# Kernel tuning notes

Hardware: AMD Instinct MI355X
Metric: run time of the kernel (lower is better)

Reference implementation:

```python
import jax, jax.numpy as jnp
import numpy as np


def setup_inputs() -> dict:
    key = jax.random.key(0)
    k1, k2 = jax.random.split(key)
    set1 = jax.random.normal(k1, (8192, 256), dtype=jnp.float32)
    set2 = jax.random.normal(k2, (8192, 256), dtype=jnp.float32)
    return {"set1": set1, "set2": set2}


def reference(set1, set2):
    # Pairwise Euclidean distances via the Gram trick:
    sq1 = jnp.sum(set1 * set1, axis=-1)  # [N]
    sq2 = jnp.sum(set2 * set2, axis=-1)  # [M]
    gram = jnp.einsum('nd,md->nm', set1, set2)  # [N,M]
    d2 = sq1[:, None] + sq2[None, :] - 2.0 * gram
    d = jnp.sqrt(jnp.maximum(d2, 0.0))  # clamp tiny negatives from roundoff
    term_1 = jnp.mean(jnp.min(d, axis=1))  # for each point in set1, nearest in set2
    term_2 = jnp.mean(jnp.min(d, axis=0))  # for each point in set2, nearest in set1
    return term_1 + term_2
```

## Files before the change

### kernel.cpp

```cpp
#include <hip/hip_runtime.h>

#define N_PTS 8192
#define D_DIM 256
#define BT 128
#define BK 32
#define INF_BITS 0x7F800000u

typedef __attribute__((ext_vector_type(8))) short short8;
typedef __attribute__((ext_vector_type(4))) float f32x4;

__device__ __forceinline__ void gload_lds16(const ushort* g, ushort* l) {
    __builtin_amdgcn_global_load_lds(
        (const __attribute__((address_space(1))) void*)g,
        (__attribute__((address_space(3))) void*)l, 16, 0, 0);
}

__device__ __forceinline__ ushort f2bf(float x) {
    unsigned u = __float_as_uint(x);
    return (ushort)((u + 0x7FFFu + ((u >> 16) & 1u)) >> 16);
}

__global__ void convert_kernel(const float* __restrict__ s1,
                               const float* __restrict__ s2,
                               ushort* __restrict__ b1,
                               ushort* __restrict__ b2) {
    const int half = N_PTS * D_DIM;
    int i = (blockIdx.x * 256 + threadIdx.x) * 8;
    const float* src; ushort* dst; int off;
    if (i < half) { src = s1; dst = b1; off = i; }
    else          { src = s2; dst = b2; off = i - half; }
    float4 v0 = *(const float4*)(src + off);
    float4 v1 = *(const float4*)(src + off + 4);
    ushort4 o0 = { f2bf(v0.x), f2bf(v0.y), f2bf(v0.z), f2bf(v0.w) };
    ushort4 o1 = { f2bf(v1.x), f2bf(v1.y), f2bf(v1.z), f2bf(v1.w) };
    *(ushort4*)(dst + off)     = o0;
    *(ushort4*)(dst + off + 4) = o1;
}

__global__ void sqnorm_kernel(const float* __restrict__ set1,
                              const float* __restrict__ set2,
                              float* __restrict__ sq1,
                              float* __restrict__ sq2) {
    int wave = threadIdx.x >> 6;
    int lane = threadIdx.x & 63;
    int row = blockIdx.x * 4 + wave;
    const float* src; float* dst; int r;
    if (row < N_PTS) { src = set1; dst = sq1; r = row; }
    else             { src = set2; dst = sq2; r = row - N_PTS; }
    float4 v = ((const float4*)(src + (size_t)r * D_DIM))[lane];
    float s = v.x * v.x + v.y * v.y + v.z * v.z + v.w * v.w;
    #pragma unroll
    for (int off = 32; off > 0; off >>= 1) s += __shfl_down(s, off, 64);
    if (lane == 0) dst[r] = s;
}

__global__ void init_kernel(unsigned int* __restrict__ rowmin2,
                            unsigned int* __restrict__ colmin2) {
    int i = blockIdx.x * blockDim.x + threadIdx.x;
    if (i < N_PTS) { rowmin2[i] = INF_BITS; colmin2[i] = INF_BITS; }
}

__global__ __launch_bounds__(256) void tile_kernel(
    const ushort* __restrict__ B1, const ushort* __restrict__ B2,
    const float* __restrict__ sq1, const float* __restrict__ sq2,
    unsigned int* __restrict__ rowmin2, unsigned int* __restrict__ colmin2) {
    __shared__ ushort As[BT * BK] __attribute__((aligned(16)));
    __shared__ ushort Bs[BT * BK] __attribute__((aligned(16)));
    __shared__ unsigned int rs[BT];
    __shared__ unsigned int cs[BT];

    const int tid  = threadIdx.x;
    const int lane = tid & 63;
    const int w    = tid >> 6;
    const int quad = lane >> 4;
    const int c    = lane & 15;
    const int n_off = (w >> 1) * 64;
    const int m_off = (w & 1) * 64;
    const int n0 = blockIdx.y * BT;
    const int m0 = blockIdx.x * BT;

    if (tid < BT) { rs[tid] = INF_BITS; cs[tid] = INF_BITS; }

    f32x4 acc[4][4];
    #pragma unroll
    for (int ti = 0; ti < 4; ti++)
        #pragma unroll
        for (int tj = 0; tj < 4; tj++) acc[ti][tj] = (f32x4){0.f, 0.f, 0.f, 0.f};

    for (int k0 = 0; k0 < D_DIM; k0 += BK) {
        #pragma unroll
        for (int ch = 0; ch < 2; ch++) {
            int idx = ch * 256 + tid;
            int row = idx >> 2;
            int c4  = idx & 3;
            gload_lds16(B1 + (size_t)(n0 + row) * D_DIM + k0 + c4 * 8,
                        &As[(idx & ~63) * 8]);
            gload_lds16(B2 + (size_t)(m0 + row) * D_DIM + k0 + c4 * 8,
                        &Bs[(idx & ~63) * 8]);
        }
        __syncthreads();

        short8 a[4], b[4];
        #pragma unroll
        for (int ti = 0; ti < 4; ti++)
            a[ti] = *(const short8*)&As[(n_off + ti * 16 + c) * BK + quad * 8];
        #pragma unroll
        for (int tj = 0; tj < 4; tj++)
            b[tj] = *(const short8*)&Bs[(m_off + tj * 16 + c) * BK + quad * 8];
        #pragma unroll
        for (int ti = 0; ti < 4; ti++)
            #pragma unroll
            for (int tj = 0; tj < 4; tj++)
                acc[ti][tj] = __builtin_amdgcn_mfma_f32_16x16x32_bf16(
                    a[ti], b[tj], acc[ti][tj], 0, 0, 0);
        __syncthreads();
    }

    float sqn[4][4], sqm[4];
    #pragma unroll
    for (int ti = 0; ti < 4; ti++)
        #pragma unroll
        for (int r = 0; r < 4; r++)
            sqn[ti][r] = sq1[n0 + n_off + ti * 16 + quad * 4 + r];
    #pragma unroll
    for (int tj = 0; tj < 4; tj++)
        sqm[tj] = sq2[m0 + m_off + tj * 16 + c];

    float rmin[4][4], cmin[4];
    #pragma unroll
    for (int ti = 0; ti < 4; ti++)
        #pragma unroll
        for (int r = 0; r < 4; r++) rmin[ti][r] = __uint_as_float(INF_BITS);
    #pragma unroll
    for (int tj = 0; tj < 4; tj++) cmin[tj] = __uint_as_float(INF_BITS);

    #pragma unroll
    for (int ti = 0; ti < 4; ti++)
        #pragma unroll
        for (int tj = 0; tj < 4; tj++)
            #pragma unroll
            for (int r = 0; r < 4; r++) {
                float d2 = fmaxf(sqn[ti][r] + sqm[tj] - 2.f * acc[ti][tj][r], 0.f);
                rmin[ti][r] = fminf(rmin[ti][r], d2);
                cmin[tj]    = fminf(cmin[tj], d2);
            }

    #pragma unroll
    for (int m = 1; m <= 8; m <<= 1)
        #pragma unroll
        for (int ti = 0; ti < 4; ti++)
            #pragma unroll
            for (int r = 0; r < 4; r++)
                rmin[ti][r] = fminf(rmin[ti][r], __shfl_xor(rmin[ti][r], m, 64));
    #pragma unroll
    for (int m = 16; m <= 32; m <<= 1)
        #pragma unroll
        for (int tj = 0; tj < 4; tj++)
            cmin[tj] = fminf(cmin[tj], __shfl_xor(cmin[tj], m, 64));

    if (c == 0) {
        #pragma unroll
        for (int ti = 0; ti < 4; ti++)
            #pragma unroll
            for (int r = 0; r < 4; r++)
                atomicMin(&rs[n_off + ti * 16 + quad * 4 + r],
                          __float_as_uint(rmin[ti][r]));
    }
    if (quad == 0) {
        #pragma unroll
        for (int tj = 0; tj < 4; tj++)
            atomicMin(&cs[m_off + tj * 16 + c], __float_as_uint(cmin[tj]));
    }
    __syncthreads();
    if (tid < BT) atomicMin(&rowmin2[n0 + tid], rs[tid]);
    else          atomicMin(&colmin2[m0 + tid - BT], cs[tid - BT]);
}

__global__ void reduce_kernel(const unsigned int* __restrict__ rowmin2,
                              const unsigned int* __restrict__ colmin2,
                              float* __restrict__ out) {
    float s = 0.f;
    for (int i = threadIdx.x; i < N_PTS; i += blockDim.x) {
        s += sqrtf(__uint_as_float(rowmin2[i]));
        s += sqrtf(__uint_as_float(colmin2[i]));
    }
    #pragma unroll
    for (int off = 32; off > 0; off >>= 1) s += __shfl_down(s, off, 64);
    __shared__ float ws[4];
    int lane = threadIdx.x & 63, wave = threadIdx.x >> 6;
    if (lane == 0) ws[wave] = s;
    __syncthreads();
    if (threadIdx.x == 0) out[0] = (ws[0] + ws[1] + ws[2] + ws[3]) / (float)N_PTS;
}

extern "C" void kernel_launch(void* const* d_in, const int* in_sizes, int n_in,
                              void* d_out, int out_size, void* d_ws, size_t ws_size,
                              hipStream_t stream) {
    const float* set1 = (const float*)d_in[0];
    const float* set2 = (const float*)d_in[1];
    float* out = (float*)d_out;

    unsigned int* rowmin2 = (unsigned int*)d_ws;
    unsigned int* colmin2 = rowmin2 + N_PTS;
    float* sq1 = (float*)(colmin2 + N_PTS);
    float* sq2 = sq1 + N_PTS;
    ushort* b1 = (ushort*)(sq2 + N_PTS);
    ushort* b2 = b1 + (size_t)N_PTS * D_DIM;

    init_kernel<<<(N_PTS + 255) / 256, 256, 0, stream>>>(rowmin2, colmin2);
    sqnorm_kernel<<<(2 * N_PTS) / 4, 256, 0, stream>>>(set1, set2, sq1, sq2);
    convert_kernel<<<(2 * N_PTS * D_DIM) / (256 * 8), 256, 0, stream>>>(
        set1, set2, b1, b2);
    tile_kernel<<<dim3(N_PTS / BT, N_PTS / BT), 256, 0, stream>>>(
        b1, b2, sq1, sq2, rowmin2, colmin2);
    reduce_kernel<<<1, 256, 0, stream>>>(rowmin2, colmin2, out);
}
```

Before: 139.7 us.

## Fuse prep kernels, enlarge swizzled GEMM tiles, fold final reduction into last block

Merges the conversion, squared-norm and min-init kernels into one prep pass, cutting launches and a second read of the fp32 inputs. The tile kernel grows to 256x128 tiles with BK=64 and an XOR-swizzled LDS layout, meant to avoid bank conflicts and raise reuse per loaded element. The separate reduce kernel is replaced by a last-block-done counter that does the final sqrt-mean inside the tile kernel. Costs are higher register pressure from 32 accumulators per wave (launch bounds set to 2 blocks) and a serial tail in the last block.

```diff
diff --git a/kernel.cpp b/kernel.cpp
--- a/kernel.cpp
+++ b/kernel.cpp
@@ -2,8 +2,10 @@
 
 #define N_PTS 8192
 #define D_DIM 256
-#define BT 128
-#define BK 32
+#define BN 256
+#define BM 128
+#define BK 64
+#define NBLK ((N_PTS / BN) * (N_PTS / BM))
 #define INF_BITS 0x7F800000u
 
 typedef __attribute__((ext_vector_type(8))) short short8;
@@ -20,177 +22,181 @@
     return (ushort)((u + 0x7FFFu + ((u >> 16) & 1u)) >> 16);
 }
 
-__global__ void convert_kernel(const float* __restrict__ s1,
-                               const float* __restrict__ s2,
-                               ushort* __restrict__ b1,
-                               ushort* __restrict__ b2) {
+__global__ void prep_kernel(const float* __restrict__ s1, const float* __restrict__ s2,
+                            ushort* __restrict__ b1, ushort* __restrict__ b2,
+                            float* __restrict__ sq1, float* __restrict__ sq2,
+                            unsigned* __restrict__ rowmin2, unsigned* __restrict__ colmin2,
+                            unsigned* __restrict__ counter) {
     const int half = N_PTS * D_DIM;
-    int i = (blockIdx.x * 256 + threadIdx.x) * 8;
-    const float* src; ushort* dst; int off;
-    if (i < half) { src = s1; dst = b1; off = i; }
-    else          { src = s2; dst = b2; off = i - half; }
+    int t = blockIdx.x * 256 + threadIdx.x;
+    int e = t * 8;
+    bool first = e < half;
+    const float* src = first ? s1 : s2;
+    ushort* dst = first ? b1 : b2;
+    int off = first ? e : e - half;
     float4 v0 = *(const float4*)(src + off);
     float4 v1 = *(const float4*)(src + off + 4);
+    float s = v0.x * v0.x + v0.y * v0.y + v0.z * v0.z + v0.w * v0.w
+            + v1.x * v1.x + v1.y * v1.y + v1.z * v1.z + v1.w * v1.w;
     ushort4 o0 = { f2bf(v0.x), f2bf(v0.y), f2bf(v0.z), f2bf(v0.w) };
     ushort4 o1 = { f2bf(v1.x), f2bf(v1.y), f2bf(v1.z), f2bf(v1.w) };
     *(ushort4*)(dst + off)     = o0;
     *(ushort4*)(dst + off + 4) = o1;
-}
-
-__global__ void sqnorm_kernel(const float* __restrict__ set1,
-                              const float* __restrict__ set2,
-                              float* __restrict__ sq1,
-                              float* __restrict__ sq2) {
-    int wave = threadIdx.x >> 6;
-    int lane = threadIdx.x & 63;
-    int row = blockIdx.x * 4 + wave;
-    const float* src; float* dst; int r;
-    if (row < N_PTS) { src = set1; dst = sq1; r = row; }
-    else             { src = set2; dst = sq2; r = row - N_PTS; }
-    float4 v = ((const float4*)(src + (size_t)r * D_DIM))[lane];
-    float s = v.x * v.x + v.y * v.y + v.z * v.z + v.w * v.w;
-    #pragma unroll
-    for (int off = 32; off > 0; off >>= 1) s += __shfl_down(s, off, 64);
-    if (lane == 0) dst[r] = s;
-}
-
-__global__ void init_kernel(unsigned int* __restrict__ rowmin2,
-                            unsigned int* __restrict__ colmin2) {
-    int i = blockIdx.x * blockDim.x + threadIdx.x;
-    if (i < N_PTS) { rowmin2[i] = INF_BITS; colmin2[i] = INF_BITS; }
-}
-
-__global__ __launch_bounds__(256) void tile_kernel(
+    #pragma unroll
+    for (int m = 1; m <= 16; m <<= 1) s += __shfl_xor(s, m, 64);
+    int sub = threadIdx.x & 31;
+    int row = off >> 8;
+    if (sub == 0) (first ? sq1 : sq2)[row] = s;
+    if (sub == 1) (first ? rowmin2 : colmin2)[row] = INF_BITS;
+    if (t == 0) *counter = 0;
+}
+
+__global__ __launch_bounds__(256, 2) void tile_kernel(
     const ushort* __restrict__ B1, const ushort* __restrict__ B2,
     const float* __restrict__ sq1, const float* __restrict__ sq2,
-    unsigned int* __restrict__ rowmin2, unsigned int* __restrict__ colmin2) {
-    __shared__ ushort As[BT * BK] __attribute__((aligned(16)));
-    __shared__ ushort Bs[BT * BK] __attribute__((aligned(16)));
-    __shared__ unsigned int rs[BT];
-    __shared__ unsigned int cs[BT];
+    unsigned* __restrict__ rowmin2, unsigned* __restrict__ colmin2,
+    unsigned* __restrict__ counter, float* __restrict__ out) {
+    __shared__ ushort As[BN * BK] __attribute__((aligned(16)));
+    __shared__ ushort Bs[BM * BK] __attribute__((aligned(16)));
+    __shared__ unsigned rs[BN];
+    __shared__ unsigned cs[BM];
+    __shared__ unsigned s_last;
+    __shared__ float wsum[4];
 
     const int tid  = threadIdx.x;
     const int lane = tid & 63;
     const int w    = tid >> 6;
     const int quad = lane >> 4;
     const int c    = lane & 15;
-    const int n_off = (w >> 1) * 64;
+    const int n_off = (w >> 1) * 128;
     const int m_off = (w & 1) * 64;
-    const int n0 = blockIdx.y * BT;
-    const int m0 = blockIdx.x * BT;
-
-    if (tid < BT) { rs[tid] = INF_BITS; cs[tid] = INF_BITS; }
-
-    f32x4 acc[4][4];
-    #pragma unroll
-    for (int ti = 0; ti < 4; ti++)
+    const int n0 = blockIdx.y * BN;
+    const int m0 = blockIdx.x * BM;
+
+    rs[tid] = INF_BITS;
+    if (tid < BM) cs[tid] = INF_BITS;
+
+    f32x4 acc[8][4];
+    #pragma unroll
+    for (int ti = 0; ti < 8; ti++)
         #pragma unroll
         for (int tj = 0; tj < 4; tj++) acc[ti][tj] = (f32x4){0.f, 0.f, 0.f, 0.f};
 
     for (int k0 = 0; k0 < D_DIM; k0 += BK) {
         #pragma unroll
-        for (int ch = 0; ch < 2; ch++) {
-            int idx = ch * 256 + tid;
-            int row = idx >> 2;
-            int c4  = idx & 3;
-            gload_lds16(B1 + (size_t)(n0 + row) * D_DIM + k0 + c4 * 8,
+        for (int r = 0; r < 8; r++) {
+            int idx = r * 256 + tid;
+            int row = idx >> 3;
+            int gc  = (idx & 7) ^ (row & 7);
+            gload_lds16(B1 + (size_t)(n0 + row) * D_DIM + k0 + gc * 8,
                         &As[(idx & ~63) * 8]);
-            gload_lds16(B2 + (size_t)(m0 + row) * D_DIM + k0 + c4 * 8,
+        }
+        #pragma unroll
+        for (int r = 0; r < 4; r++) {
+            int idx = r * 256 + tid;
+            int row = idx >> 3;
+            int gc  = (idx & 7) ^ (row & 7);
+            gload_lds16(B2 + (size_t)(m0 + row) * D_DIM + k0 + gc * 8,
                         &Bs[(idx & ~63) * 8]);
         }
         __syncthreads();
 
-        short8 a[4], b[4];
-        #pragma unroll
-        for (int ti = 0; ti < 4; ti++)
-            a[ti] = *(const short8*)&As[(n_off + ti * 16 + c) * BK + quad * 8];
-        #pragma unroll
-        for (int tj = 0; tj < 4; tj++)
-            b[tj] = *(const short8*)&Bs[(m_off + tj * 16 + c) * BK + quad * 8];
-        #pragma unroll
-        for (int ti = 0; ti < 4; ti++)
-            #pragma unroll
-            for (int tj = 0; tj < 4; tj++)
-                acc[ti][tj] = __builtin_amdgcn_mfma_f32_16x16x32_bf16(
-                    a[ti], b[tj], acc[ti][tj], 0, 0, 0);
+        #pragma unroll
+        for (int kk = 0; kk < 2; kk++) {
+            short8 a[8], b[4];
+            #pragma unroll
+            for (int ti = 0; ti < 8; ti++) {
+                int row = n_off + ti * 16 + c;
+                int ch  = (kk * 4 + quad) ^ (row & 7);
+                a[ti] = *(const short8*)&As[row * BK + ch * 8];
+            }
+            #pragma unroll
+            for (int tj = 0; tj < 4; tj++) {
+                int row = m_off + tj * 16 + c;
+                int ch  = (kk * 4 + quad) ^ (row & 7);
+                b[tj] = *(const short8*)&Bs[row * BK + ch * 8];
+            }
+            #pragma unroll
+            for (int ti = 0; ti < 8; ti++)
+                #pragma unroll
+                for (int tj = 0; tj < 4; tj++)
+                    acc[ti][tj] = __builtin_amdgcn_mfma_f32_16x16x32_bf16(
+                        a[ti], b[tj], acc[ti][tj], 0, 0, 0);
+        }
         __syncthreads();
     }
 
-    float sqn[4][4], sqm[4];
-    #pragma unroll
-    for (int ti = 0; ti < 4; ti++)
-        #pragma unroll
-        for (int r = 0; r < 4; r++)
-            sqn[ti][r] = sq1[n0 + n_off + ti * 16 + quad * 4 + r];
-    #pragma unroll
-    for (int tj = 0; tj < 4; tj++)
-        sqm[tj] = sq2[m0 + m_off + tj * 16 + c];
-
-    float rmin[4][4], cmin[4];
-    #pragma unroll
-    for (int ti = 0; ti < 4; ti++)
-        #pragma unroll
-        for (int r = 0; r < 4; r++) rmin[ti][r] = __uint_as_float(INF_BITS);
+    float sqm[4];
+    #pragma unroll
+    for (int tj = 0; tj < 4; tj++) sqm[tj] = sq2[m0 + m_off + tj * 16 + c];
+    float cmin[4];
     #pragma unroll
     for (int tj = 0; tj < 4; tj++) cmin[tj] = __uint_as_float(INF_BITS);
 
     #pragma unroll
-    for (int ti = 0; ti < 4; ti++)
-        #pragma unroll
-        for (int tj = 0; tj < 4; tj++)
+    for (int ti = 0; ti < 8; ti++) {
+        float4 sqn = *(const float4*)&sq1[n0 + n_off + ti * 16 + quad * 4];
+        float rmin[4] = { __uint_as_float(INF_BITS), __uint_as_float(INF_BITS),
+                          __uint_as_float(INF_BITS), __uint_as_float(INF_BITS) };
+        #pragma unroll
+        for (int tj = 0; tj < 4; tj++) {
+            float sn[4] = { sqn.x, sqn.y, sqn.z, sqn.w };
             #pragma unroll
             for (int r = 0; r < 4; r++) {
-                float d2 = fmaxf(sqn[ti][r] + sqm[tj] - 2.f * acc[ti][tj][r], 0.f);
-                rmin[ti][r] = fminf(rmin[ti][r], d2);
-                cmin[tj]    = fminf(cmin[tj], d2);
+                float d2 = fmaxf(sn[r] + sqm[tj] - 2.f * acc[ti][tj][r], 0.f);
+                rmin[r]  = fminf(rmin[r], d2);
+                cmin[tj] = fminf(cmin[tj], d2);
             }
-
-    #pragma unroll
-    for (int m = 1; m <= 8; m <<= 1)
-        #pragma unroll
-        for (int ti = 0; ti < 4; ti++)
+        }
+        #pragma unroll
+        for (int m = 1; m <= 8; m <<= 1)
             #pragma unroll
             for (int r = 0; r < 4; r++)
-                rmin[ti][r] = fminf(rmin[ti][r], __shfl_xor(rmin[ti][r], m, 64));
+                rmin[r] = fminf(rmin[r], __shfl_xor(rmin[r], m, 64));
+        if (c == 0) {
+            #pragma unroll
+            for (int r = 0; r < 4; r++)
+                atomicMin(&rs[n_off + ti * 16 + quad * 4 + r], __float_as_uint(rmin[r]));
+        }
+    }
     #pragma unroll
     for (int m = 16; m <= 32; m <<= 1)
         #pragma unroll
         for (int tj = 0; tj < 4; tj++)
             cmin[tj] = fminf(cmin[tj], __shfl_xor(cmin[tj], m, 64));
-
-    if (c == 0) {
-        #pragma unroll
-        for (int ti = 0; ti < 4; ti++)
-            #pragma unroll
-            for (int r = 0; r < 4; r++)
-                atomicMin(&rs[n_off + ti * 16 + quad * 4 + r],
-                          __float_as_uint(rmin[ti][r]));
-    }
     if (quad == 0) {
         #pragma unroll
         for (int tj = 0; tj < 4; tj++)
             atomicMin(&cs[m_off + tj * 16 + c], __float_as_uint(cmin[tj]));
     }
     __syncthreads();
-    if (tid < BT) atomicMin(&rowmin2[n0 + tid], rs[tid]);
-    else          atomicMin(&colmin2[m0 + tid - BT], cs[tid - BT]);
-}
-
-__global__ void reduce_kernel(const unsigned int* __restrict__ rowmin2,
-                              const unsigned int* __restrict__ colmin2,
-                              float* __restrict__ out) {
-    float s = 0.f;
-    for (int i = threadIdx.x; i < N_PTS; i += blockDim.x) {
-        s += sqrtf(__uint_as_float(rowmin2[i]));
-        s += sqrtf(__uint_as_float(colmin2[i]));
-    }
-    #pragma unroll
-    for (int off = 32; off > 0; off >>= 1) s += __shfl_down(s, off, 64);
-    __shared__ float ws[4];
-    int lane = threadIdx.x & 63, wave = threadIdx.x >> 6;
-    if (lane == 0) ws[wave] = s;
+
+    atomicMin(&rowmin2[n0 + tid], rs[tid]);
+    if (tid < BM) atomicMin(&colmin2[m0 + tid], cs[tid]);
+
+    __threadfence();
     __syncthreads();
-    if (threadIdx.x == 0) out[0] = (ws[0] + ws[1] + ws[2] + ws[3]) / (float)N_PTS;
+    if (tid == 0) s_last = (atomicAdd(counter, 1) == NBLK - 1) ? 1u : 0u;
+    __syncthreads();
+    if (s_last) {
+        __threadfence();
+        const unsigned* mins = rowmin2;
+        float s = 0.f;
+        for (int base = 0; base < 2 * N_PTS; base += 2048) {
+            unsigned v[8];
+            #pragma unroll
+            for (int j = 0; j < 8; j++)
+                v[j] = __hip_atomic_load(&mins[base + j * 256 + tid],
+                                         __ATOMIC_RELAXED, __HIP_MEMORY_SCOPE_AGENT);
+            #pragma unroll
+            for (int j = 0; j < 8; j++) s += sqrtf(__uint_as_float(v[j]));
+        }
+        #pragma unroll
+        for (int off = 32; off > 0; off >>= 1) s += __shfl_down(s, off, 64);
+        if (lane == 0) wsum[w] = s;
+        __syncthreads();
+        if (tid == 0) out[0] = (wsum[0] + wsum[1] + wsum[2] + wsum[3]) / (float)N_PTS;
+    }
 }
 
 extern "C" void kernel_launch(void* const* d_in, const int* in_sizes, int n_in,
@@ -200,18 +206,16 @@
     const float* set2 = (const float*)d_in[1];
     float* out = (float*)d_out;
 
-    unsigned int* rowmin2 = (unsigned int*)d_ws;
-    unsigned int* colmin2 = rowmin2 + N_PTS;
+    unsigned* rowmin2 = (unsigned*)d_ws;
+    unsigned* colmin2 = rowmin2 + N_PTS;
     float* sq1 = (float*)(colmin2 + N_PTS);
     float* sq2 = sq1 + N_PTS;
-    ushort* b1 = (ushort*)(sq2 + N_PTS);
+    unsigned* counter = (unsigned*)(sq2 + N_PTS);
+    ushort* b1 = (ushort*)((char*)d_ws + 128 * 1024);
     ushort* b2 = b1 + (size_t)N_PTS * D_DIM;
 
-    init_kernel<<<(N_PTS + 255) / 256, 256, 0, stream>>>(rowmin2, colmin2);
-    sqnorm_kernel<<<(2 * N_PTS) / 4, 256, 0, stream>>>(set1, set2, sq1, sq2);
-    convert_kernel<<<(2 * N_PTS * D_DIM) / (256 * 8), 256, 0, stream>>>(
-        set1, set2, b1, b2);
-    tile_kernel<<<dim3(N_PTS / BT, N_PTS / BT), 256, 0, stream>>>(
-        b1, b2, sq1, sq2, rowmin2, colmin2);
-    reduce_kernel<<<1, 256, 0, stream>>>(rowmin2, colmin2, out);
-}
+    prep_kernel<<<(2 * N_PTS * D_DIM) / (256 * 8), 256, 0, stream>>>(
+        set1, set2, b1, b2, sq1, sq2, rowmin2, colmin2, counter);
+    tile_kernel<<<dim3(N_PTS / BM, N_PTS / BN), 256, 0, stream>>>(
+        b1, b2, sq1, sq2, rowmin2, colmin2, counter, out);
+}
```

Result: slower. 238.7 us (+70.8%).
